# Performance work log

Hardware: AMD Instinct MI355X
Metric: run time of the kernel (lower is better)

## Reference

```python
import jax, jax.numpy as jnp
import numpy as np

MIN_C = 1e-6
MIN_NORM = 1e-15
BALL_EPS = 0.004  # float32 ball epsilon


def _norm(x):
    return jnp.maximum(jnp.linalg.norm(x, axis=-1, keepdims=True), MIN_NORM)


def _project(x, c):
    norm = _norm(x)
    maxnorm = (1.0 - BALL_EPS) / jnp.sqrt(c)
    return jnp.where(norm > maxnorm, x / norm * maxnorm, x)


def _tanh(x):
    return jnp.tanh(jnp.clip(x, -15.0, 15.0))


def _artanh(x):
    x = jnp.clip(x, -1.0 + 1e-5, 1.0 - 1e-5)
    return 0.5 * (jnp.log1p(x) - jnp.log1p(-x))


def _expmap0(u, c):
    sc = jnp.sqrt(c)
    n = _norm(u)
    return _project(_tanh(sc * n) * u / (sc * n), c)


def _logmap0(y, c):
    sc = jnp.sqrt(c)
    n = _norm(y)
    return y / n / sc * _artanh(sc * n)


def _mobius_add(x, y, c):
    x2 = jnp.sum(x * x, -1, keepdims=True)
    y2 = jnp.sum(y * y, -1, keepdims=True)
    xy = jnp.sum(x * y, -1, keepdims=True)
    num = (1 + 2 * c * xy + c * y2) * x + (1 - c * x2) * y
    den = jnp.maximum(1 + 2 * c * xy + c * c * x2 * y2, MIN_NORM)
    return num / den


N_NODE, N_EDGE, D, ATTN, B, N_VOCAB = 100000, 1000000, 64, 64, 256, 401


def setup_inputs() -> dict:
    key = jax.random.key(0)
    ks = jax.random.split(key, 12)
    r_idx = jax.random.randint(ks[0], (N_EDGE,), 0, B, dtype=jnp.int32)
    rel = jax.random.randint(ks[1], (N_EDGE,), 0, N_VOCAB, dtype=jnp.int32)
    sub = jax.random.randint(ks[2], (N_EDGE,), 0, N_NODE, dtype=jnp.int32)
    obj = jax.random.randint(ks[3], (N_EDGE,), 0, N_NODE, dtype=jnp.int32)
    zero = jnp.zeros((N_EDGE,), jnp.int32)
    edges = jnp.stack([r_idx, zero, rel, zero, sub, obj], axis=1)  # [E, 6]
    s = 0.1
    return {
        "hidden": jax.random.normal(ks[4], (N_NODE, D), jnp.float32) * s,
        "q_rel": jax.random.randint(ks[5], (B,), 0, N_VOCAB, dtype=jnp.int32),
        "edges": edges,
        "rela_embed": jax.random.normal(ks[6], (N_VOCAB, D), jnp.float32) * s,
        "Ws_w": jax.random.normal(ks[7], (ATTN, D), jnp.float32) * s,
        "Wr_w": jax.random.normal(ks[8], (ATTN, D), jnp.float32) * s,
        "Wqr_w": jax.random.normal(ks[9], (ATTN, D), jnp.float32) * s,
        "Wqr_b": jnp.zeros((ATTN,), jnp.float32),
        "Wattn_w": jax.random.normal(ks[10], (1, ATTN), jnp.float32) * s,
        "Wh_w": jax.random.normal(ks[11], (D, D), jnp.float32) * s,
        "n_node": N_NODE,
    }


def reference(hidden, q_rel, edges, rela_embed, Ws_w, Wr_w, Wqr_w, Wqr_b, Wattn_w, Wh_w, n_node):
    c = MIN_C
    sub, rel, obj, r_idx = edges[:, 4], edges[:, 2], edges[:, 5], edges[:, 0]
    hs = hidden[sub]                 # [E, D] gather
    hr = rela_embed[rel]             # [E, D]
    h_qr = rela_embed[q_rel][r_idx]  # [E, D]
    # attention MLP -> scalar gate per edge
    pre = hs @ Ws_w.T + hr @ Wr_w.T + h_qr @ Wqr_w.T + Wqr_b
    alpha = jax.nn.sigmoid(jax.nn.relu(pre) @ Wattn_w.T)  # [E, 1]
    # hyperbolic message
    hs_h = _expmap0(hs, c)
    hr_h = _expmap0(hr, c)
    mess2 = _logmap0(_project(_mobius_add(hs_h, hr_h, c), c), c)
    message = mess2 * alpha
    agg = jax.ops.segment_sum(message, obj, num_segments=n_node)  # scatter-add
    a = _expmap0(agg @ Wh_w.T, c)
    a = jax.nn.relu(a)  # act
    return _logmap0(a, c)
```

## Files before the change

### kernel.cpp

```cpp
#include <hip/hip_runtime.h>
#include <math.h>
#include <stdint.h>

#define N_NODE 100000
#define N_EDGE 1000000
#define DIM    64
#define NB     256
#define NVOCAB 401
#define SCAN_B 1024
#define NCHUNK ((N_NODE + SCAN_B - 1) / SCAN_B)
#define AGG_WAVES 8192
#define NSHARD 8
#define EPB 2048

typedef short short8  __attribute__((ext_vector_type(8)));
typedef float floatx4 __attribute__((ext_vector_type(4)));
typedef unsigned short ushort_t;

__device__ inline unsigned short f2bf_rne(float f)
{
    unsigned u = __float_as_uint(f);
    unsigned r = u + 0x7FFF + ((u >> 16) & 1);
    return (unsigned short)(r >> 16);
}
__device__ inline float bflo(unsigned u) { return __uint_as_float(u << 16); }
__device__ inline float bfhi(unsigned u) { return __uint_as_float(u & 0xFFFF0000u); }
__device__ inline unsigned short f2h(float f)
{
    _Float16 h = (_Float16)f;
    unsigned short s; __builtin_memcpy(&s, &h, 2); return s;
}
__device__ inline float h2f(unsigned b)
{
    unsigned short s = (unsigned short)b;
    _Float16 h; __builtin_memcpy(&h, &s, 2); return (float)h;
}

__device__ inline void split8(float4 v0, float4 v1, short8& hi, short8& lo)
{
    float f[8] = {v0.x, v0.y, v0.z, v0.w, v1.x, v1.y, v1.z, v1.w};
    #pragma unroll
    for (int j = 0; j < 8; ++j) {
        unsigned u = __float_as_uint(f[j]);
        unsigned r = u + 0x7FFF + ((u >> 16) & 1);
        unsigned short h = (unsigned short)(r >> 16);
        float hf = __uint_as_float(((unsigned)h) << 16);
        float l  = f[j] - hf;
        unsigned u2 = __float_as_uint(l);
        unsigned r2 = u2 + 0x7FFF + ((u2 >> 16) & 1);
        hi[j] = (short)h;
        lo[j] = (short)(r2 >> 16);
    }
}

#define INIT_GRID ((NSHARD * N_NODE + 255) / 256)

__global__ __launch_bounds__(256) void init_kernel(
    const float* __restrict__ Ws, const float* __restrict__ Wr,
    const float* __restrict__ Wqr, const float* __restrict__ Wh,
    ushort_t* __restrict__ wsp, int* __restrict__ deg8)
{
    int tid = blockIdx.x * 256 + threadIdx.x;
    if (tid < NSHARD * N_NODE) deg8[tid] = 0;
    if (tid < 4 * 4096) {
        int w = tid >> 12, e = tid & 4095;
        const float* src = (w == 0) ? Ws : (w == 1) ? Wr : (w == 2) ? Wqr : Wh;
        float f = src[e];
        unsigned u = __float_as_uint(f);
        unsigned r = u + 0x7FFF + ((u >> 16) & 1);
        unsigned short h = (unsigned short)(r >> 16);
        float hf = __uint_as_float(((unsigned)h) << 16);
        float l  = f - hf;
        unsigned u2 = __float_as_uint(l);
        unsigned r2 = u2 + 0x7FFF + ((u2 >> 16) & 1);
        wsp[w * 8192 + e]        = h;
        wsp[w * 8192 + 4096 + e] = (unsigned short)(r2 >> 16);
    }
}

__device__ void gemm64p_body(
    const float* __restrict__ X,
    const int*   __restrict__ idx,
    const ushort_t* __restrict__ Whi,
    const ushort_t* __restrict__ Wlo,
    const float* __restrict__ bias,
    void* __restrict__ Yv,
    ushort_t* __restrict__ Y2,
    int R, int out_mode, int blk)
{
    int wave = threadIdx.x >> 6;
    int lane = threadIdx.x & 63;
    int m    = lane & 15;
    int quad = lane >> 4;
    int r0   = blk * 64 + wave * 16;

    int r = r0 + m;
    int src = (r < R) ? (idx ? idx[r] : r) : 0;
    const float* xrow = X + (size_t)src * DIM + quad * 8;

    float4 a0[2], a1[2];
    #pragma unroll
    for (int c = 0; c < 2; ++c) {
        a0[c] = *(const float4*)(xrow + 32 * c);
        a1[c] = *(const float4*)(xrow + 32 * c + 4);
    }
    short8 ah[2], al[2];
    #pragma unroll
    for (int c = 0; c < 2; ++c) split8(a0[c], a1[c], ah[c], al[c]);

    if (out_mode == 3 && r < R) {
        #pragma unroll
        for (int c = 0; c < 2; ++c)
            *(short8*)(Y2 + (size_t)r * DIM + 32 * c + quad * 8) = ah[c];
    }

    floatx4 acc[4] = {{0,0,0,0},{0,0,0,0},{0,0,0,0},{0,0,0,0}};
    #pragma unroll
    for (int g = 0; g < 4; ++g) {
        const ushort_t* whrow = Whi + (size_t)(g * 16 + m) * DIM + quad * 8;
        const ushort_t* wlrow = Wlo + (size_t)(g * 16 + m) * DIM + quad * 8;
        #pragma unroll
        for (int c = 0; c < 2; ++c) {
            short8 bh = *(const short8*)(whrow + 32 * c);
            short8 bl = *(const short8*)(wlrow + 32 * c);
            acc[g] = __builtin_amdgcn_mfma_f32_16x16x32_bf16(bh, ah[c], acc[g], 0, 0, 0);
            acc[g] = __builtin_amdgcn_mfma_f32_16x16x32_bf16(bl, ah[c], acc[g], 0, 0, 0);
            acc[g] = __builtin_amdgcn_mfma_f32_16x16x32_bf16(bh, al[c], acc[g], 0, 0, 0);
        }
    }

    if (r < R) {
        #pragma unroll
        for (int g = 0; g < 4; ++g) {
            float4 bv = make_float4(0.f, 0.f, 0.f, 0.f);
            if (bias) bv = *(const float4*)(bias + g * 16 + quad * 4);
            float v0 = acc[g][0] + bv.x;
            float v1 = acc[g][1] + bv.y;
            float v2 = acc[g][2] + bv.z;
            float v3 = acc[g][3] + bv.w;
            if (out_mode == 1) {
                v0 = fmaxf(v0, 0.f); v1 = fmaxf(v1, 0.f);
                v2 = fmaxf(v2, 0.f); v3 = fmaxf(v3, 0.f);
            }
            if (out_mode >= 2) {
                uint2 o;
                o.x = (unsigned)f2bf_rne(v0) | ((unsigned)f2bf_rne(v1) << 16);
                o.y = (unsigned)f2bf_rne(v2) | ((unsigned)f2bf_rne(v3) << 16);
                *(uint2*)((ushort_t*)Yv + (size_t)r * DIM + g * 16 + quad * 4) = o;
            } else {
                *(float4*)((float*)Yv + (size_t)r * DIM + g * 16 + quad * 4) =
                    make_float4(v0, v1, v2, v3);
            }
        }
    }
}

__global__ __launch_bounds__(256) void gemm64p_bf16A_kernel(
    const ushort_t* __restrict__ A,
    const ushort_t* __restrict__ Whi,
    const ushort_t* __restrict__ Wlo,
    float* __restrict__ Y, int R)
{
    int wave = threadIdx.x >> 6;
    int lane = threadIdx.x & 63;
    int m    = lane & 15;
    int quad = lane >> 4;
    int r0   = blockIdx.x * 64 + wave * 16;

    int r = r0 + m;
    int src = (r < R) ? r : 0;
    short8 a8[2];
    #pragma unroll
    for (int c = 0; c < 2; ++c)
        a8[c] = *(const short8*)(A + (size_t)src * DIM + 32 * c + quad * 8);

    floatx4 acc[4] = {{0,0,0,0},{0,0,0,0},{0,0,0,0},{0,0,0,0}};
    #pragma unroll
    for (int g = 0; g < 4; ++g) {
        const ushort_t* whrow = Whi + (size_t)(g * 16 + m) * DIM + quad * 8;
        const ushort_t* wlrow = Wlo + (size_t)(g * 16 + m) * DIM + quad * 8;
        #pragma unroll
        for (int c = 0; c < 2; ++c) {
            short8 bh = *(const short8*)(whrow + 32 * c);
            short8 bl = *(const short8*)(wlrow + 32 * c);
            acc[g] = __builtin_amdgcn_mfma_f32_16x16x32_bf16(bh, a8[c], acc[g], 0, 0, 0);
            acc[g] = __builtin_amdgcn_mfma_f32_16x16x32_bf16(bl, a8[c], acc[g], 0, 0, 0);
        }
    }

    if (r < R) {
        #pragma unroll
        for (int g = 0; g < 4; ++g) {
            *(float4*)(Y + (size_t)r * DIM + g * 16 + quad * 4) =
                make_float4(fmaxf(acc[g][0], 0.f), fmaxf(acc[g][1], 0.f),
                            fmaxf(acc[g][2], 0.f), fmaxf(acc[g][3], 0.f));
        }
    }
}

__device__ void gemm64_body(
    const float* __restrict__ X,
    const int*   __restrict__ idx,
    const float* __restrict__ W,
    const float* __restrict__ bias,
    void* __restrict__ Yv,
    ushort_t* __restrict__ Y2,
    int R, int out_mode, int blk)
{
    int wave = threadIdx.x >> 6;
    int lane = threadIdx.x & 63;
    int m    = lane & 15;
    int quad = lane >> 4;
    int r0   = blk * 64 + wave * 16;

    int r = r0 + m;
    int src = (r < R) ? (idx ? idx[r] : r) : 0;
    const float* xrow = X + (size_t)src * DIM + quad * 8;

    float4 a0[2], a1[2];
    #pragma unroll
    for (int c = 0; c < 2; ++c) {
        a0[c] = *(const float4*)(xrow + 32 * c);
        a1[c] = *(const float4*)(xrow + 32 * c + 4);
    }
    short8 ah[2], al[2];
    #pragma unroll
    for (int c = 0; c < 2; ++c) split8(a0[c], a1[c], ah[c], al[c]);

    if (out_mode == 3 && r < R) {
        #pragma unroll
        for (int c = 0; c < 2; ++c)
            *(short8*)(Y2 + (size_t)r * DIM + 32 * c + quad * 8) = ah[c];
    }

    floatx4 acc[4] = {{0,0,0,0},{0,0,0,0},{0,0,0,0},{0,0,0,0}};
    #pragma unroll
    for (int g = 0; g < 4; ++g) {
        const float* wrow = W + (size_t)(g * 16 + m) * DIM + quad * 8;
        #pragma unroll
        for (int c = 0; c < 2; ++c) {
            float4 b0 = *(const float4*)(wrow + 32 * c);
            float4 b1 = *(const float4*)(wrow + 32 * c + 4);
            short8 bh, bl;
            split8(b0, b1, bh, bl);
            acc[g] = __builtin_amdgcn_mfma_f32_16x16x32_bf16(ah[c], bh, acc[g], 0, 0, 0);
            acc[g] = __builtin_amdgcn_mfma_f32_16x16x32_bf16(ah[c], bl, acc[g], 0, 0, 0);
            acc[g] = __builtin_amdgcn_mfma_f32_16x16x32_bf16(al[c], bh, acc[g], 0, 0, 0);
        }
    }

    #pragma unroll
    for (int g = 0; g < 4; ++g) {
        float bv = bias ? bias[g * 16 + m] : 0.0f;
        #pragma unroll
        for (int reg = 0; reg < 4; ++reg) {
            int rr = r0 + quad * 4 + reg;
            if (rr < R) {
                float v = acc[g][reg] + bv;
                if (out_mode == 1) v = fmaxf(v, 0.0f);
                if (out_mode >= 2)
                    ((ushort_t*)Yv)[(size_t)rr * DIM + g * 16 + m] = f2bf_rne(v);
                else
                    ((float*)Yv)[(size_t)rr * DIM + g * 16 + m] = v;
            }
        }
    }
}

__global__ __launch_bounds__(256) void gemm64_kernel(
    const float* __restrict__ X, const int* __restrict__ idx,
    const float* __restrict__ W, const float* __restrict__ bias,
    void* __restrict__ Yv, ushort_t* __restrict__ Y2, int R, int out_mode)
{
    gemm64_body(X, idx, W, bias, Yv, Y2, R, out_mode, blockIdx.x);
}

#define G1 ((N_NODE + 63) / 64)
#define G2 ((NVOCAB + 63) / 64)
#define G3 (NB / 64)
#define GSMALL (G2 + G3)
#define GD8 ((N_EDGE + EPB - 1) / EPB)
#define PREP_T (G1 + GD8)
#define PREP_GRID (GSMALL + PREP_T)

__global__ __launch_bounds__(256) void prep_kernel(
    const float* __restrict__ hidden,
    const float* __restrict__ rela,
    const int*   __restrict__ q_rel,
    const ushort_t* __restrict__ wsp,
    const float* __restrict__ Wqr_b,
    ushort_t* __restrict__ hsWs,
    ushort_t* __restrict__ hidb,
    ushort_t* __restrict__ rel_preb,
    ushort_t* __restrict__ relab,
    ushort_t* __restrict__ qr_preb,
    const int* __restrict__ edges,
    int* __restrict__ deg8,
    int* __restrict__ rank,
    int2* __restrict__ epack)
{
    int b = blockIdx.x;
    if (b < G2) {
        gemm64p_body(rela, nullptr, wsp + 1 * 8192, wsp + 1 * 8192 + 4096,
                     nullptr, rel_preb, relab, NVOCAB, 3, b);
    } else if (b < GSMALL) {
        gemm64p_body(rela, q_rel, wsp + 2 * 8192, wsp + 2 * 8192 + 4096,
                     Wqr_b, qr_preb, nullptr, NB, 2, b - G2);
    } else {
        int bp = b - GSMALL;
        int prior = (int)(((long)bp * GD8) / PREP_T);
        int nxt   = (int)(((long)(bp + 1) * GD8) / PREP_T);
        if (nxt > prior) {
            int base = prior * EPB + threadIdx.x;
            #pragma unroll
            for (int k = 0; k < 8; ++k) {
                int e = base + k * 256;
                if (e < N_EDGE) {
                    int2 ab = *(const int2*)(edges + (size_t)e * 6);
                    int2 cd = *(const int2*)(edges + (size_t)e * 6 + 2);
                    int2 ef = *(const int2*)(edges + (size_t)e * 6 + 4);
                    epack[e] = make_int2(ef.x | (cd.x << 17), ef.y | (ab.x << 17));
                    int s = (e >> 11) & (NSHARD - 1);
                    rank[e] = atomicAdd(&deg8[s * N_NODE + ef.y], 1);
                }
            }
        } else {
            gemm64p_body(hidden, nullptr, wsp, wsp + 4096,
                         nullptr, hsWs, hidb, N_NODE, 3, bp - prior);
        }
    }
}

__global__ __launch_bounds__(SCAN_B) void scan1_kernel(const int* __restrict__ deg8,
                                                       int* __restrict__ partial)
{
    __shared__ int s[SCAN_B];
    int g = blockIdx.x * SCAN_B + threadIdx.x;
    int tot = 0;
    if (g < N_NODE)
        #pragma unroll
        for (int k = 0; k < NSHARD; ++k) tot += deg8[k * N_NODE + g];
    s[threadIdx.x] = tot;
    __syncthreads();
    for (int off = SCAN_B / 2; off; off >>= 1) {
        if (threadIdx.x < off) s[threadIdx.x] += s[threadIdx.x + off];
        __syncthreads();
    }
    if (threadIdx.x == 0) partial[blockIdx.x] = s[0];
}

__global__ __launch_bounds__(128) void scan2_kernel(int* __restrict__ partial, int n)
{
    __shared__ int s[128];
    int t = threadIdx.x;
    int v = (t < n) ? partial[t] : 0;
    s[t] = v;
    __syncthreads();
    for (int off = 1; off < 128; off <<= 1) {
        int add = (t >= off) ? s[t - off] : 0;
        __syncthreads();
        s[t] += add;
        __syncthreads();
    }
    if (t < n) partial[t] = s[t] - v;
}

__global__ __launch_bounds__(SCAN_B) void scan3_kernel(int* __restrict__ deg8,
                                                       const int* __restrict__ partial,
                                                       int* __restrict__ offs)
{
    __shared__ int s[SCAN_B];
    int g = blockIdx.x * SCAN_B + threadIdx.x;
    int d[NSHARD];
    int tot = 0;
    if (g < N_NODE) {
        #pragma unroll
        for (int k = 0; k < NSHARD; ++k) { d[k] = deg8[k * N_NODE + g]; tot += d[k]; }
    }
    s[threadIdx.x] = tot;
    __syncthreads();
    for (int off = 1; off < SCAN_B; off <<= 1) {
        int add = ((int)threadIdx.x >= off) ? s[threadIdx.x - off] : 0;
        __syncthreads();
        s[threadIdx.x] += add;
        __syncthreads();
    }
    if (g < N_NODE) {
        int incl = partial[blockIdx.x] + s[threadIdx.x];
        offs[g + 1] = incl;
        if (g == 0) offs[0] = 0;
        int run = incl - tot;
        #pragma unroll
        for (int k = 0; k < NSHARD; ++k) { deg8[k * N_NODE + g] = run; run += d[k]; }
    }
}

__global__ __launch_bounds__(256) void alpha_scatter_kernel(
    const int2*     __restrict__ epack,
    const int*      __restrict__ rank,
    const int*      __restrict__ base8,
    const ushort_t* __restrict__ hsWs,
    const ushort_t* __restrict__ rel_preb,
    const ushort_t* __restrict__ qr_preb,
    const float*    __restrict__ wattn,
    int2*           __restrict__ csr2)
{
    int tid = blockIdx.x * 256 + threadIdx.x;
    if (tid < 4) csr2[N_EDGE + tid] = make_int2(0, 0);

    int wave = threadIdx.x >> 6;
    int lane = threadIdx.x & 63;
    int q    = lane >> 4;
    int l    = lane & 15;
    int f0   = l * 4;
    int e0   = (blockIdx.x * 4 + wave) * 16 + q * 4;

    float4 wa = *(const float4*)(wattn + f0);

    int   sub[4], rl[4], ob[4];
    float t[4];
    #pragma unroll
    for (int j = 0; j < 4; ++j) {
        int e = e0 + j;
        int2 ep = epack[e];
        sub[j] = ep.x & 0x1FFFF;
        rl[j]  = (int)((unsigned)ep.x >> 17);
        ob[j]  = ep.y & 0x1FFFF;
        int ri = (int)((unsigned)ep.y >> 17);

        uint2 uh = *(const uint2*)(hsWs     + (size_t)sub[j] * DIM + f0);
        uint2 ur = *(const uint2*)(rel_preb + (size_t)rl[j]  * DIM + f0);
        uint2 uq = *(const uint2*)(qr_preb  + (size_t)ri     * DIM + f0);

        float tt =  fmaxf(bflo(uh.x) + bflo(ur.x) + bflo(uq.x), 0.f) * wa.x;
        tt = fmaf(fmaxf(bfhi(uh.x) + bfhi(ur.x) + bfhi(uq.x), 0.f), wa.y, tt);
        tt = fmaf(fmaxf(bflo(uh.y) + bflo(ur.y) + bflo(uq.y), 0.f), wa.z, tt);
        tt = fmaf(fmaxf(bfhi(uh.y) + bfhi(ur.y) + bfhi(uq.y), 0.f), wa.w, tt);
        t[j] = tt;
    }
    #pragma unroll
    for (int j = 0; j < 4; ++j) {
        t[j] += __shfl_xor(t[j], 1);
        t[j] += __shfl_xor(t[j], 2);
        t[j] += __shfl_xor(t[j], 4);
        t[j] += __shfl_xor(t[j], 8);
    }

    if (l < 4) {
        int j = l;
        int sh = (e0 >> 11) & (NSHARD - 1);
        float alpha = 1.0f / (1.0f + __expf(-t[j]));
        int slot = base8[sh * N_NODE + ob[j]] + rank[e0 + j];
        csr2[slot] = make_int2(sub[j],
            (int)(((unsigned)rl[j] << 16) | f2h(alpha)));
    }
}

__global__ __launch_bounds__(256) void agg_kernel(
    const int2*     __restrict__ csr2,
    const int*      __restrict__ offs,
    const ushort_t* __restrict__ hB,
    const ushort_t* __restrict__ relab,
    ushort_t* __restrict__ aggb)
{
    int lane = threadIdx.x & 63;
    int q    = lane >> 4;
    int l    = lane & 15;
    int f0   = l * 4;
    int wv = __builtin_amdgcn_readfirstlane((blockIdx.x * blockDim.x + threadIdx.x) >> 6);

    int i   = offs[wv];
    int end = offs[wv + 1];
    for (int n = wv; n < N_NODE; n += AGG_WAVES) {
        int nn = n + AGG_WAVES;
        int ni = 0, ne = 0;
        if (nn < N_NODE) { ni = offs[nn]; ne = offs[nn + 1]; }

        float4 acc = make_float4(0.f, 0.f, 0.f, 0.f);
        int2 e0 = csr2[min(i + q,     N_EDGE + 3)];
        int2 e1 = csr2[min(i + 4 + q, N_EDGE + 3)];
        while (i < end) {
            int2 f0e = csr2[min(i + 8 + q,  N_EDGE + 3)];
            int2 f1e = csr2[min(i + 12 + q, N_EDGE + 3)];
            float v0 = (i + q < end)     ? 1.0f : 0.0f;
            float v1 = (i + 4 + q < end) ? 1.0f : 0.0f;

            unsigned ey0 = (unsigned)e0.y, ey1 = (unsigned)e1.y;
            float al0 = v0 * h2f(ey0 & 0xFFFFu);
            float al1 = v1 * h2f(ey1 & 0xFFFFu);

            uint2 uh0 = *(const uint2*)(hB    + (size_t)e0.x        * DIM + f0);
            uint2 ur0 = *(const uint2*)(relab + (size_t)(ey0 >> 16) * DIM + f0);
            uint2 uh1 = *(const uint2*)(hB    + (size_t)e1.x        * DIM + f0);
            uint2 ur1 = *(const uint2*)(relab + (size_t)(ey1 >> 16) * DIM + f0);

            acc.x = fmaf(al0, bflo(uh0.x) + bflo(ur0.x), acc.x);
            acc.y = fmaf(al0, bfhi(uh0.x) + bfhi(ur0.x), acc.y);
            acc.z = fmaf(al0, bflo(uh0.y) + bflo(ur0.y), acc.z);
            acc.w = fmaf(al0, bfhi(uh0.y) + bfhi(ur0.y), acc.w);
            acc.x = fmaf(al1, bflo(uh1.x) + bflo(ur1.x), acc.x);
            acc.y = fmaf(al1, bfhi(uh1.x) + bfhi(ur1.x), acc.y);
            acc.z = fmaf(al1, bflo(uh1.y) + bflo(ur1.y), acc.z);
            acc.w = fmaf(al1, bfhi(uh1.y) + bfhi(ur1.y), acc.w);

            e0 = f0e; e1 = f1e;
            i += 8;
        }

        acc.x += __shfl_xor(acc.x, 16); acc.x += __shfl_xor(acc.x, 32);
        acc.y += __shfl_xor(acc.y, 16); acc.y += __shfl_xor(acc.y, 32);
        acc.z += __shfl_xor(acc.z, 16); acc.z += __shfl_xor(acc.z, 32);
        acc.w += __shfl_xor(acc.w, 16); acc.w += __shfl_xor(acc.w, 32);
        if (q == 0) {
            uint2 o;
            o.x = (unsigned)f2bf_rne(acc.x) | ((unsigned)f2bf_rne(acc.y) << 16);
            o.y = (unsigned)f2bf_rne(acc.z) | ((unsigned)f2bf_rne(acc.w) << 16);
            *(uint2*)(aggb + (size_t)n * DIM + f0) = o;
        }

        i = ni; end = ne;
    }
}

__global__ __launch_bounds__(256) void edge_kernel(
    const int*      __restrict__ edges,
    const ushort_t* __restrict__ hB,
    const ushort_t* __restrict__ relab,
    const ushort_t* __restrict__ hsWs,
    const ushort_t* __restrict__ rel_preb,
    const ushort_t* __restrict__ qr_preb,
    const float*    __restrict__ wattn,
    float* __restrict__ out)
{
    int e = (blockIdx.x * blockDim.x + threadIdx.x) >> 6;
    if (e >= N_EDGE) return;
    int lane = threadIdx.x & 63;
    int r_i = edges[e * 6 + 0];
    int rl  = edges[e * 6 + 2];
    int sb  = edges[e * 6 + 4];
    int ob  = edges[e * 6 + 5];
    float hs = __uint_as_float(((unsigned)hB[(size_t)sb * DIM + lane]) << 16);
    float hr = __uint_as_float(((unsigned)relab[(size_t)rl * DIM + lane]) << 16);
    float p1 = __uint_as_float(((unsigned)hsWs[(size_t)sb * DIM + lane]) << 16);
    float p2 = __uint_as_float(((unsigned)rel_preb[(size_t)rl * DIM + lane]) << 16);
    float p3 = __uint_as_float(((unsigned)qr_preb[(size_t)r_i * DIM + lane]) << 16);
    float t = wattn[lane] * fmaxf(p1 + p2 + p3, 0.0f);
    #pragma unroll
    for (int off = 32; off; off >>= 1) t += __shfl_xor(t, off);
    float alpha = 1.0f / (1.0f + __expf(-t));
    atomicAdd(&out[(size_t)ob * DIM + lane], (hs + hr) * alpha);
}

extern "C" void kernel_launch(void* const* d_in, const int* in_sizes, int n_in,
                              void* d_out, int out_size, void* d_ws, size_t ws_size,
                              hipStream_t stream)
{
    const float* hidden = (const float*)d_in[0];
    const int*   q_rel  = (const int*)  d_in[1];
    const int*   edges  = (const int*)  d_in[2];
    const float* rela   = (const float*)d_in[3];
    const float* Ws     = (const float*)d_in[4];
    const float* Wr     = (const float*)d_in[5];
    const float* Wqr    = (const float*)d_in[6];
    const float* Wqr_b  = (const float*)d_in[7];
    const float* Wattn  = (const float*)d_in[8];
    const float* Wh     = (const float*)d_in[9];
    float* out = (float*)d_out;

    ushort_t* qr_preb  = (ushort_t*)d_ws;
    ushort_t* rel_preb = qr_preb + NB * DIM;
    ushort_t* relab    = rel_preb + NVOCAB * DIM;
    ushort_t* hsWs     = relab + NVOCAB * DIM;
    ushort_t* hidb     = hsWs + (size_t)N_NODE * DIM;
    int2* epack  = (int2*)(((uintptr_t)(hidb + (size_t)N_NODE * DIM) + 15) & ~(uintptr_t)15);
    int*  rank   = (int*)(epack + N_EDGE);
    int*  deg8   = rank + N_EDGE;
    int*  offs   = deg8 + NSHARD * N_NODE;
    int*  partial= offs + (N_NODE + 1);
    int2* csr2   = (int2*)(((uintptr_t)(partial + 128) + 15) & ~(uintptr_t)15);
    ushort_t* wsp = (ushort_t*)(csr2 + N_EDGE + 4);
    size_t csr_need = ((char*)(wsp + 4 * 8192)) - (char*)d_ws;
    bool use_csr = ws_size >= csr_need;
    ushort_t* aggb = (ushort_t*)epack;

    if (use_csr) {
        init_kernel<<<INIT_GRID, 256, 0, stream>>>(Ws, Wr, Wqr, Wh, wsp, deg8);
        prep_kernel<<<PREP_GRID, 256, 0, stream>>>(
            hidden, rela, q_rel, wsp, Wqr_b,
            hsWs, hidb, rel_preb, relab, qr_preb, edges, deg8, rank, epack);
        scan1_kernel<<<NCHUNK, SCAN_B, 0, stream>>>(deg8, partial);
        scan2_kernel<<<1, 128, 0, stream>>>(partial, NCHUNK);
        scan3_kernel<<<NCHUNK, SCAN_B, 0, stream>>>(deg8, partial, offs);
        alpha_scatter_kernel<<<N_EDGE / 64, 256, 0, stream>>>(
            epack, rank, deg8, hsWs, rel_preb, qr_preb, Wattn, csr2);
        agg_kernel<<<AGG_WAVES / 4, 256, 0, stream>>>(csr2, offs, hidb, relab, aggb);
        gemm64p_bf16A_kernel<<<(N_NODE + 63) / 64, 256, 0, stream>>>(
            aggb, wsp + 3 * 8192, wsp + 3 * 8192 + 4096, out, N_NODE);
    } else {
        gemm64_kernel<<<(NVOCAB + 63) / 64, 256, 0, stream>>>(
            rela, nullptr, Wr, nullptr, rel_preb, relab, NVOCAB, 3);
        gemm64_kernel<<<(NB + 63) / 64, 256, 0, stream>>>(
            rela, q_rel, Wqr, Wqr_b, qr_preb, nullptr, NB, 2);
        gemm64_kernel<<<(N_NODE + 63) / 64, 256, 0, stream>>>(
            hidden, nullptr, Ws, nullptr, hsWs, hidb, N_NODE, 3);
        hipMemsetAsync(d_out, 0, (size_t)N_NODE * DIM * sizeof(float), stream);
        edge_kernel<<<(N_EDGE + 3) / 4, 256, 0, stream>>>(
            edges, hidb, relab, hsWs, rel_preb, qr_preb, Wattn, out);
        gemm64_kernel<<<(N_NODE + 63) / 64, 256, 0, stream>>>(
            out, nullptr, Wh, nullptr, out, nullptr, N_NODE, 1);
    }
}
```

Before: 262.6 us.

## Give each degree-count shard to one workgroup using workgroup-scope atomics

```diff
diff --git a/kernel.cpp b/kernel.cpp
--- a/kernel.cpp
+++ b/kernel.cpp
@@ -10,8 +10,8 @@
 #define SCAN_B 1024
 #define NCHUNK ((N_NODE + SCAN_B - 1) / SCAN_B)
 #define AGG_WAVES 8192
-#define NSHARD 8
-#define EPB 2048
+#define NSHARD 32
+#define DEG_E (N_EDGE / NSHARD)
 
 typedef short short8  __attribute__((ext_vector_type(8)));
 typedef float floatx4 __attribute__((ext_vector_type(4)));
@@ -53,15 +53,14 @@
     }
 }
 
-#define INIT_GRID ((NSHARD * N_NODE + 255) / 256)
+#define INIT_GRID ((4 * 4096 + 255) / 256)
 
 __global__ __launch_bounds__(256) void init_kernel(
     const float* __restrict__ Ws, const float* __restrict__ Wr,
     const float* __restrict__ Wqr, const float* __restrict__ Wh,
-    ushort_t* __restrict__ wsp, int* __restrict__ deg8)
+    ushort_t* __restrict__ wsp)
 {
     int tid = blockIdx.x * 256 + threadIdx.x;
-    if (tid < NSHARD * N_NODE) deg8[tid] = 0;
     if (tid < 4 * 4096) {
         int w = tid >> 12, e = tid & 4095;
         const float* src = (w == 0) ? Ws : (w == 1) ? Wr : (w == 2) ? Wqr : Wh;
@@ -279,9 +278,7 @@
 #define G2 ((NVOCAB + 63) / 64)
 #define G3 (NB / 64)
 #define GSMALL (G2 + G3)
-#define GD8 ((N_EDGE + EPB - 1) / EPB)
-#define PREP_T (G1 + GD8)
-#define PREP_GRID (GSMALL + PREP_T)
+#define PREP_GRID (NSHARD + GSMALL + G1)
 
 __global__ __launch_bounds__(256) void prep_kernel(
     const float* __restrict__ hidden,
@@ -300,34 +297,36 @@
     int2* __restrict__ epack)
 {
     int b = blockIdx.x;
-    if (b < G2) {
-        gemm64p_body(rela, nullptr, wsp + 1 * 8192, wsp + 1 * 8192 + 4096,
-                     nullptr, rel_preb, relab, NVOCAB, 3, b);
-    } else if (b < GSMALL) {
-        gemm64p_body(rela, q_rel, wsp + 2 * 8192, wsp + 2 * 8192 + 4096,
-                     Wqr_b, qr_preb, nullptr, NB, 2, b - G2);
-    } else {
-        int bp = b - GSMALL;
-        int prior = (int)(((long)bp * GD8) / PREP_T);
-        int nxt   = (int)(((long)(bp + 1) * GD8) / PREP_T);
-        if (nxt > prior) {
-            int base = prior * EPB + threadIdx.x;
+    if (b < NSHARD) {
+        int* mydeg = deg8 + (size_t)b * N_NODE;
+        for (int g = threadIdx.x * 4; g < N_NODE; g += 256 * 4)
+            *(int4*)(mydeg + g) = make_int4(0, 0, 0, 0);
+        __syncthreads();
+        int base = b * DEG_E;
+        for (int e0i = 0; e0i < DEG_E; e0i += 2048) {
             #pragma unroll
             for (int k = 0; k < 8; ++k) {
-                int e = base + k * 256;
-                if (e < N_EDGE) {
+                int off = e0i + k * 256 + threadIdx.x;
+                if (off < DEG_E) {
+                    int e = base + off;
                     int2 ab = *(const int2*)(edges + (size_t)e * 6);
                     int2 cd = *(const int2*)(edges + (size_t)e * 6 + 2);
                     int2 ef = *(const int2*)(edges + (size_t)e * 6 + 4);
                     epack[e] = make_int2(ef.x | (cd.x << 17), ef.y | (ab.x << 17));
-                    int s = (e >> 11) & (NSHARD - 1);
-                    rank[e] = atomicAdd(&deg8[s * N_NODE + ef.y], 1);
+                    rank[e] = __hip_atomic_fetch_add(&mydeg[ef.y], 1,
+                                  __ATOMIC_RELAXED, __HIP_MEMORY_SCOPE_WORKGROUP);
                 }
             }
-        } else {
-            gemm64p_body(hidden, nullptr, wsp, wsp + 4096,
-                         nullptr, hsWs, hidb, N_NODE, 3, bp - prior);
-        }
+        }
+    } else if (b < NSHARD + G2) {
+        gemm64p_body(rela, nullptr, wsp + 1 * 8192, wsp + 1 * 8192 + 4096,
+                     nullptr, rel_preb, relab, NVOCAB, 3, b - NSHARD);
+    } else if (b < NSHARD + GSMALL) {
+        gemm64p_body(rela, q_rel, wsp + 2 * 8192, wsp + 2 * 8192 + 4096,
+                     Wqr_b, qr_preb, nullptr, NB, 2, b - NSHARD - G2);
+    } else {
+        gemm64p_body(hidden, nullptr, wsp, wsp + 4096,
+                     nullptr, hsWs, hidb, N_NODE, 3, b - NSHARD - GSMALL);
     }
 }
 
@@ -339,7 +338,7 @@
     int tot = 0;
     if (g < N_NODE)
         #pragma unroll
-        for (int k = 0; k < NSHARD; ++k) tot += deg8[k * N_NODE + g];
+        for (int k = 0; k < NSHARD; ++k) tot += deg8[(size_t)k * N_NODE + g];
     s[threadIdx.x] = tot;
     __syncthreads();
     for (int off = SCAN_B / 2; off; off >>= 1) {
@@ -375,7 +374,7 @@
     int tot = 0;
     if (g < N_NODE) {
         #pragma unroll
-        for (int k = 0; k < NSHARD; ++k) { d[k] = deg8[k * N_NODE + g]; tot += d[k]; }
+        for (int k = 0; k < NSHARD; ++k) { d[k] = deg8[(size_t)k * N_NODE + g]; tot += d[k]; }
     }
     s[threadIdx.x] = tot;
     __syncthreads();
@@ -391,7 +390,7 @@
         if (g == 0) offs[0] = 0;
         int run = incl - tot;
         #pragma unroll
-        for (int k = 0; k < NSHARD; ++k) { deg8[k * N_NODE + g] = run; run += d[k]; }
+        for (int k = 0; k < NSHARD; ++k) { deg8[(size_t)k * N_NODE + g] = run; run += d[k]; }
     }
 }
 
@@ -448,9 +447,10 @@
 
     if (l < 4) {
         int j = l;
-        int sh = (e0 >> 11) & (NSHARD - 1);
+        int e = e0 + j;
+        int sh = (int)((unsigned)e / (unsigned)DEG_E);
         float alpha = 1.0f / (1.0f + __expf(-t[j]));
-        int slot = base8[sh * N_NODE + ob[j]] + rank[e0 + j];
+        int slot = base8[(size_t)sh * N_NODE + ob[j]] + rank[e];
         csr2[slot] = make_int2(sub[j],
             (int)(((unsigned)rl[j] << 16) | f2h(alpha)));
     }
@@ -575,7 +575,7 @@
     int2* epack  = (int2*)(((uintptr_t)(hidb + (size_t)N_NODE * DIM) + 15) & ~(uintptr_t)15);
     int*  rank   = (int*)(epack + N_EDGE);
     int*  deg8   = rank + N_EDGE;
-    int*  offs   = deg8 + NSHARD * N_NODE;
+    int*  offs   = deg8 + (size_t)NSHARD * N_NODE;
     int*  partial= offs + (N_NODE + 1);
     int2* csr2   = (int2*)(((uintptr_t)(partial + 128) + 15) & ~(uintptr_t)15);
     ushort_t* wsp = (ushort_t*)(csr2 + N_EDGE + 4);
@@ -584,7 +584,7 @@
     ushort_t* aggb = (ushort_t*)epack;
 
     if (use_csr) {
-        init_kernel<<<INIT_GRID, 256, 0, stream>>>(Ws, Wr, Wqr, Wh, wsp, deg8);
+        init_kernel<<<INIT_GRID, 256, 0, stream>>>(Ws, Wr, Wqr, Wh, wsp);
         prep_kernel<<<PREP_GRID, 256, 0, stream>>>(
             hidden, rela, q_rel, wsp, Wqr_b,
             hsWs, hidb, rel_preb, relab, qr_preb, edges, deg8, rank, epack);
```

After: 363.2 us. 38.3% more time.

## Fuse scan2 into scan3 and unroll agg gather loop to 16 edges

Applied to the files above, without the earlier changes.

```diff
diff --git a/kernel.cpp b/kernel.cpp
--- a/kernel.cpp
+++ b/kernel.cpp
@@ -349,27 +349,24 @@
     if (threadIdx.x == 0) partial[blockIdx.x] = s[0];
 }
 
-__global__ __launch_bounds__(128) void scan2_kernel(int* __restrict__ partial, int n)
-{
-    __shared__ int s[128];
-    int t = threadIdx.x;
-    int v = (t < n) ? partial[t] : 0;
-    s[t] = v;
-    __syncthreads();
-    for (int off = 1; off < 128; off <<= 1) {
-        int add = (t >= off) ? s[t - off] : 0;
-        __syncthreads();
-        s[t] += add;
-        __syncthreads();
-    }
-    if (t < n) partial[t] = s[t] - v;
-}
-
 __global__ __launch_bounds__(SCAN_B) void scan3_kernel(int* __restrict__ deg8,
                                                        const int* __restrict__ partial,
                                                        int* __restrict__ offs)
 {
     __shared__ int s[SCAN_B];
+    __shared__ int pbase_s;
+    int pb = (threadIdx.x < (int)blockIdx.x) ? partial[threadIdx.x] : 0;
+    s[threadIdx.x] = pb;
+    __syncthreads();
+    for (int off = SCAN_B / 2; off; off >>= 1) {
+        if (threadIdx.x < off) s[threadIdx.x] += s[threadIdx.x + off];
+        __syncthreads();
+    }
+    if (threadIdx.x == 0) pbase_s = s[0];
+    __syncthreads();
+    int pbase = pbase_s;
+    __syncthreads();
+
     int g = blockIdx.x * SCAN_B + threadIdx.x;
     int d[NSHARD];
     int tot = 0;
@@ -386,7 +383,7 @@
         __syncthreads();
     }
     if (g < N_NODE) {
-        int incl = partial[blockIdx.x] + s[threadIdx.x];
+        int incl = pbase + s[threadIdx.x];
         offs[g + 1] = incl;
         if (g == 0) offs[0] = 0;
         int run = incl - tot;
@@ -406,7 +403,7 @@
     int2*           __restrict__ csr2)
 {
     int tid = blockIdx.x * 256 + threadIdx.x;
-    if (tid < 4) csr2[N_EDGE + tid] = make_int2(0, 0);
+    if (tid < 32) csr2[N_EDGE + tid] = make_int2(0, 0);
 
     int wave = threadIdx.x >> 6;
     int lane = threadIdx.x & 63;
@@ -448,9 +445,10 @@
 
     if (l < 4) {
         int j = l;
+        int e = e0 + j;
         int sh = (e0 >> 11) & (NSHARD - 1);
         float alpha = 1.0f / (1.0f + __expf(-t[j]));
-        int slot = base8[sh * N_NODE + ob[j]] + rank[e0 + j];
+        int slot = base8[sh * N_NODE + ob[j]] + rank[e];
         csr2[slot] = make_int2(sub[j],
             (int)(((unsigned)rl[j] << 16) | f2h(alpha)));
     }
@@ -477,34 +475,34 @@
         if (nn < N_NODE) { ni = offs[nn]; ne = offs[nn + 1]; }
 
         float4 acc = make_float4(0.f, 0.f, 0.f, 0.f);
-        int2 e0 = csr2[min(i + q,     N_EDGE + 3)];
-        int2 e1 = csr2[min(i + 4 + q, N_EDGE + 3)];
+        int2 e[4];
+        #pragma unroll
+        for (int j = 0; j < 4; ++j) e[j] = csr2[i + 4 * j + q];
         while (i < end) {
-            int2 f0e = csr2[min(i + 8 + q,  N_EDGE + 3)];
-            int2 f1e = csr2[min(i + 12 + q, N_EDGE + 3)];
-            float v0 = (i + q < end)     ? 1.0f : 0.0f;
-            float v1 = (i + 4 + q < end) ? 1.0f : 0.0f;
-
-            unsigned ey0 = (unsigned)e0.y, ey1 = (unsigned)e1.y;
-            float al0 = v0 * h2f(ey0 & 0xFFFFu);
-            float al1 = v1 * h2f(ey1 & 0xFFFFu);
-
-            uint2 uh0 = *(const uint2*)(hB    + (size_t)e0.x        * DIM + f0);
-            uint2 ur0 = *(const uint2*)(relab + (size_t)(ey0 >> 16) * DIM + f0);
-            uint2 uh1 = *(const uint2*)(hB    + (size_t)e1.x        * DIM + f0);
-            uint2 ur1 = *(const uint2*)(relab + (size_t)(ey1 >> 16) * DIM + f0);
-
-            acc.x = fmaf(al0, bflo(uh0.x) + bflo(ur0.x), acc.x);
-            acc.y = fmaf(al0, bfhi(uh0.x) + bfhi(ur0.x), acc.y);
-            acc.z = fmaf(al0, bflo(uh0.y) + bflo(ur0.y), acc.z);
-            acc.w = fmaf(al0, bfhi(uh0.y) + bfhi(ur0.y), acc.w);
-            acc.x = fmaf(al1, bflo(uh1.x) + bflo(ur1.x), acc.x);
-            acc.y = fmaf(al1, bfhi(uh1.x) + bfhi(ur1.x), acc.y);
-            acc.z = fmaf(al1, bflo(uh1.y) + bflo(ur1.y), acc.z);
-            acc.w = fmaf(al1, bfhi(uh1.y) + bfhi(ur1.y), acc.w);
-
-            e0 = f0e; e1 = f1e;
-            i += 8;
+            int2 p[4];
+            #pragma unroll
+            for (int j = 0; j < 4; ++j) p[j] = csr2[i + 16 + 4 * j + q];
+
+            uint2 uh[4], ur[4];
+            #pragma unroll
+            for (int j = 0; j < 4; ++j) {
+                unsigned ey = (unsigned)e[j].y;
+                uh[j] = *(const uint2*)(hB    + (((unsigned)e[j].x) << 6) + f0);
+                ur[j] = *(const uint2*)(relab + ((ey >> 16) << 6) + f0);
+            }
+            #pragma unroll
+            for (int j = 0; j < 4; ++j) {
+                unsigned ey = (unsigned)e[j].y;
+                float v  = (i + 4 * j + q < end) ? 1.0f : 0.0f;
+                float al = v * h2f(ey & 0xFFFFu);
+                acc.x = fmaf(al, bflo(uh[j].x) + bflo(ur[j].x), acc.x);
+                acc.y = fmaf(al, bfhi(uh[j].x) + bfhi(ur[j].x), acc.y);
+                acc.z = fmaf(al, bflo(uh[j].y) + bflo(ur[j].y), acc.z);
+                acc.w = fmaf(al, bfhi(uh[j].y) + bfhi(ur[j].y), acc.w);
+            }
+            #pragma unroll
+            for (int j = 0; j < 4; ++j) e[j] = p[j];
+            i += 16;
         }
 
         acc.x += __shfl_xor(acc.x, 16); acc.x += __shfl_xor(acc.x, 32);
@@ -515,7 +513,7 @@
             uint2 o;
             o.x = (unsigned)f2bf_rne(acc.x) | ((unsigned)f2bf_rne(acc.y) << 16);
             o.y = (unsigned)f2bf_rne(acc.z) | ((unsigned)f2bf_rne(acc.w) << 16);
-            *(uint2*)(aggb + (size_t)n * DIM + f0) = o;
+            *(uint2*)(aggb + (((unsigned)n) << 6) + f0) = o;
         }
 
         i = ni; end = ne;
@@ -578,7 +576,7 @@
     int*  offs   = deg8 + NSHARD * N_NODE;
     int*  partial= offs + (N_NODE + 1);
     int2* csr2   = (int2*)(((uintptr_t)(partial + 128) + 15) & ~(uintptr_t)15);
-    ushort_t* wsp = (ushort_t*)(csr2 + N_EDGE + 4);
+    ushort_t* wsp = (ushort_t*)(csr2 + N_EDGE + 32);
     size_t csr_need = ((char*)(wsp + 4 * 8192)) - (char*)d_ws;
     bool use_csr = ws_size >= csr_need;
     ushort_t* aggb = (ushort_t*)epack;
@@ -589,7 +587,6 @@
             hidden, rela, q_rel, wsp, Wqr_b,
             hsWs, hidb, rel_preb, relab, qr_preb, edges, deg8, rank, epack);
         scan1_kernel<<<NCHUNK, SCAN_B, 0, stream>>>(deg8, partial);
-        scan2_kernel<<<1, 128, 0, stream>>>(partial, NCHUNK);
         scan3_kernel<<<NCHUNK, SCAN_B, 0, stream>>>(deg8, partial, offs);
         alpha_scatter_kernel<<<N_EDGE / 64, 256, 0, stream>>>(
             epack, rank, deg8, hsWs, rel_preb, qr_preb, Wattn, csr2);
```

New measurement: 259.2 us. About the same (-1.3%).
